# Kernel tuning notes

Hardware: AMD Instinct MI355X
Metric: run time of the kernel (lower is better)

The kernel has to match this reference:

```python
import jax, jax.numpy as jnp
import numpy as np

HD_DIM = 4096
BUNDLE_SIZE = 128
STRIDE = 128  # bundle_size - overlap, overlap = 0
EPS = 1e-8


def setup_inputs() -> dict:
    key = jax.random.key(0)
    k1, k2 = jax.random.split(key)
    inputs = jax.random.normal(k1, (4, 2048, HD_DIM), dtype=jnp.float32)
    # base vector ~ N(0, 1/sqrt(hd_dim)) as in RandomNormal(stddev=1/sqrt(hd_dim))
    base = jax.random.normal(k2, (HD_DIM,), dtype=jnp.float32) / jnp.sqrt(jnp.float32(HD_DIM))
    # position_weights initialized to decay_rate**i
    pos_w = jnp.power(jnp.float32(0.99), jnp.arange(BUNDLE_SIZE, dtype=jnp.float32))
    return {"inputs": inputs, "bundle_position_base": base, "position_weights": pos_w}


def reference(inputs, bundle_position_base, position_weights):
    B, S, D = inputs.shape
    nb = (S - BUNDLE_SIZE) // STRIDE + 1  # number of bundles

    # Cyclic-shift position vectors: pos[s, d] = base[(d - s) mod D]
    shifts = jnp.arange(BUNDLE_SIZE)
    idx = jnp.mod(jnp.arange(D)[None, :] - shifts[:, None], D)  # [bs, D]
    pos = bundle_position_base[idx]                              # [bs, D]
    w = jax.nn.softmax(position_weights)                         # [bs]
    pos = pos * w[:, None]

    # overlap=0 and S divisible by bundle_size -> bundles tile the sequence
    tok = inputs.reshape(B, nb, BUNDLE_SIZE, D)  # [B, nb, bs, D]

    # circular correlation: real(ifft(fft(tok) * conj(fft(pos))))
    # both operands real -> use rfft/irfft (identical math, half the work)
    tok_f = jnp.fft.rfft(tok, axis=-1)                 # [B, nb, bs, D//2+1]
    pos_f = jnp.conj(jnp.fft.rfft(pos, axis=-1))       # [bs, D//2+1]
    bound = jnp.fft.irfft(tok_f * pos_f[None, None], n=D, axis=-1)  # [B, nb, bs, D]

    bundle = jnp.sum(bound, axis=2)  # [B, nb, D]
    # tf.nn.l2_normalize: x * rsqrt(max(sum(x^2), eps))
    ssq = jnp.sum(bundle * bundle, axis=-1, keepdims=True)
    return (bundle * jax.lax.rsqrt(jnp.maximum(ssq, EPS))).astype(jnp.float32)
```

## Files before the change

kernel.cpp:

```cpp
#include <hip/hip_runtime.h>

#define D 4096
#define DM 4095
#define BS 128
#define NROW 64
#define QC 16
#define JC 8

#define ZSTR 520
#define PSTR 616

typedef __attribute__((ext_vector_type(8))) short bf16x8;
typedef __attribute__((ext_vector_type(4))) float f32x4;

__device__ __forceinline__ unsigned short f2bf(float f) {
  union { float f; unsigned int u; } v;
  v.f = f;
  const unsigned int r = v.u + 0x7fffu + ((v.u >> 16) & 1u);
  return (unsigned short)(r >> 16);
}

__global__ __launch_bounds__(256) void shift_k(const float* __restrict__ tok,
                                               const float* __restrict__ pw,
                                               float* __restrict__ part) {
  const int t = threadIdx.x;
  const int qc = blockIdx.x;
  const int row = blockIdx.y;

  __shared__ float wsh[BS];
  __shared__ float red[4];
  {
    const float v = (t < BS) ? pw[t] : -1e30f;
    float m = v;
#pragma unroll
    for (int o = 32; o > 0; o >>= 1) m = fmaxf(m, __shfl_xor(m, o));
    if ((t & 63) == 0) red[t >> 6] = m;
    __syncthreads();
    m = fmaxf(fmaxf(red[0], red[1]), fmaxf(red[2], red[3]));
    const float e = (t < BS) ? expf(v - m) : 0.f;
    float s = e;
#pragma unroll
    for (int o = 32; o > 0; o >>= 1) s += __shfl_xor(s, o);
    __syncthreads();
    if ((t & 63) == 0) red[t >> 6] = s;
    __syncthreads();
    s = red[0] + red[1] + red[2] + red[3];
    if (t < BS) wsh[t] = e / s;
    __syncthreads();
  }
  float wv[8];
#pragma unroll
  for (int j = 0; j < 8; ++j) wv[j] = wsh[(qc << 3) + j];

  const float4* tr = (const float4*)(tok + (size_t)row * (BS * D));
  float4 acc[4];
#pragma unroll
  for (int g = 0; g < 4; ++g) acc[g] = make_float4(0.f, 0.f, 0.f, 0.f);

#pragma unroll
  for (int qq = 0; qq < 2; ++qq) {
    const int q = (qc << 1) + qq;
    const float w0 = wv[4 * qq + 0], w1 = wv[4 * qq + 1];
    const float w2 = wv[4 * qq + 2], w3 = wv[4 * qq + 3];
#pragma unroll
    for (int g = 0; g < 4; ++g) {
      const int G = (t + (g << 8) + q) & 1023;
      const int G1 = (G + 1) & 1023;
      const size_t r0 = (size_t)(4 * q + 0) << 10;
      const size_t r1 = (size_t)(4 * q + 1) << 10;
      const size_t r2 = (size_t)(4 * q + 2) << 10;
      const size_t r3 = (size_t)(4 * q + 3) << 10;
      const float4 a0 = tr[r0 + G];
      const float4 a1 = tr[r1 + G], b1 = tr[r1 + G1];
      const float4 a2 = tr[r2 + G], b2 = tr[r2 + G1];
      const float4 a3 = tr[r3 + G], b3 = tr[r3 + G1];
      acc[g].x += w0 * a0.x; acc[g].y += w0 * a0.y;
      acc[g].z += w0 * a0.z; acc[g].w += w0 * a0.w;
      acc[g].x += w1 * a1.y; acc[g].y += w1 * a1.z;
      acc[g].z += w1 * a1.w; acc[g].w += w1 * b1.x;
      acc[g].x += w2 * a2.z; acc[g].y += w2 * a2.w;
      acc[g].z += w2 * b2.x; acc[g].w += w2 * b2.y;
      acc[g].x += w3 * a3.w; acc[g].y += w3 * b3.x;
      acc[g].z += w3 * b3.y; acc[g].w += w3 * b3.z;
    }
  }
  float4* pz = (float4*)(part + (size_t)(qc * NROW + row) * D);
#pragma unroll
  for (int g = 0; g < 4; ++g) pz[t + (g << 8)] = acc[g];
}

__global__ __launch_bounds__(256) void z_k(const float* __restrict__ part,
                                           unsigned short* __restrict__ zb) {
  const int t = threadIdx.x;
  const int mq = blockIdx.x;
  const int row = blockIdx.y;
  const int m0 = (mq << 10) + (t << 2);
  float4 s = make_float4(0.f, 0.f, 0.f, 0.f);
#pragma unroll
  for (int cc = 0; cc < QC; ++cc) {
    const float4 v = *(const float4*)(part + (size_t)(cc * NROW + row) * D + m0);
    s.x += v.x; s.y += v.y; s.z += v.z; s.w += v.w;
  }
  ushort4 o;
  o.x = f2bf(s.x); o.y = f2bf(s.y); o.z = f2bf(s.z); o.w = f2bf(s.w);
  *(ushort4*)(zb + (size_t)row * D + m0) = o;
}

__global__ __launch_bounds__(256) void corr_k(const unsigned short* __restrict__ zb,
                                              const float* __restrict__ base,
                                              float* __restrict__ braw) {
  __shared__ __align__(16) unsigned short zsh[16 * ZSTR];
  __shared__ __align__(16) unsigned short psh[8 * PSTR];
  const int t = threadIdx.x;
  const int jc = blockIdx.x;
  const int dg = blockIdx.y;
  const int rt = blockIdx.z;
  const int jb = jc << 9;
  const int d0b = dg << 6;

  {
    const int rr = t >> 4;
    const int c0 = (t & 15) << 5;
    const uint4* src =
        (const uint4*)(zb + (size_t)(rt * 16 + rr) * D + jb + c0);
    uint4* dst = (uint4*)(zsh + rr * ZSTR + c0);
    dst[0] = src[0];
    dst[1] = src[1];
    dst[2] = src[2];
    dst[3] = src[3];
  }
  {
    const int c0 = jb - d0b - 64 + 2 * D;
    for (int idx = t; idx < 8 * PSTR; idx += 256) {
      const int r = idx / PSTR;
      const int x = idx - r * PSTR;
      psh[idx] = f2bf(base[(c0 + r + x) & DM]);
    }
  }
  __syncthreads();

  const int lane = t & 63;
  const int w = t >> 6;
  const int dd = lane & 15;
  const int q = lane >> 4;
  const int a0 = 64 + (q << 3) - (w << 4) - dd;
  const int pr = a0 & 7;
  const int px = a0 - pr;
  const unsigned short* pA = psh + pr * PSTR + px;
  const unsigned short* pB = zsh + dd * ZSTR + (q << 3);

  f32x4 acc = {0.f, 0.f, 0.f, 0.f};
#pragma unroll
  for (int ks = 0; ks < 16; ++ks) {
    const bf16x8 af = *(const bf16x8*)(pA + (ks << 5));
    const bf16x8 bf = *(const bf16x8*)(pB + (ks << 5));
    acc = __builtin_amdgcn_mfma_f32_16x16x32_bf16(af, bf, acc, 0, 0, 0);
  }
  const int row = rt * 16 + dd;
  const int d = d0b + (w << 4) + (q << 2);
  float4 o = make_float4(acc[0], acc[1], acc[2], acc[3]);
  *(float4*)(braw + (size_t)(jc * NROW + row) * D + d) = o;
}

__global__ __launch_bounds__(1024) void norm_k(const float* __restrict__ braw,
                                               float* __restrict__ out) {
  const int t = threadIdx.x;
  const int row = blockIdx.x;
  const float4* b4 = (const float4*)braw;
  float4 s = make_float4(0.f, 0.f, 0.f, 0.f);
#pragma unroll
  for (int p = 0; p < JC; ++p) {
    const float4 v = b4[(size_t)(p * NROW + row) * (D / 4) + t];
    s.x += v.x; s.y += v.y; s.z += v.z; s.w += v.w;
  }
  float ssq = s.x * s.x + s.y * s.y + s.z * s.z + s.w * s.w;
#pragma unroll
  for (int o = 32; o > 0; o >>= 1) ssq += __shfl_xor(ssq, o);
  __shared__ float red[16];
  if ((t & 63) == 0) red[t >> 6] = ssq;
  __syncthreads();
  float tot = 0.f;
#pragma unroll
  for (int i = 0; i < 16; ++i) tot += red[i];
  const float sc = rsqrtf(fmaxf(tot, 1e-8f));
  float4 o;
  o.x = s.x * sc; o.y = s.y * sc; o.z = s.z * sc; o.w = s.w * sc;
  ((float4*)out)[(size_t)row * (D / 4) + t] = o;
}

extern "C" void kernel_launch(void* const* d_in, const int* in_sizes, int n_in,
                              void* d_out, int out_size, void* d_ws, size_t ws_size,
                              hipStream_t stream) {
  (void)in_sizes; (void)n_in; (void)out_size; (void)ws_size;
  const float* tok = (const float*)d_in[0];
  const float* base = (const float*)d_in[1];
  const float* pw = (const float*)d_in[2];
  float* out = (float*)d_out;

  float* part = (float*)d_ws;
  float* braw = part + (size_t)QC * NROW * D;
  unsigned short* zb =
      (unsigned short*)(braw + (size_t)JC * NROW * D);

  shift_k<<<dim3(QC, NROW), 256, 0, stream>>>(tok, pw, part);
  z_k<<<dim3(4, NROW), 256, 0, stream>>>(part, zb);
  corr_k<<<dim3(JC, 64, 4), 256, 0, stream>>>(zb, base, braw);
  norm_k<<<NROW, 1024, 0, stream>>>(braw, out);
}
```

Measured before the change: 208.5 us.

## Fuse shift-sum and partial reduction into one kernel with in-block LDS reduce

```diff
diff --git a/kernel.cpp b/kernel.cpp
--- a/kernel.cpp
+++ b/kernel.cpp
@@ -4,7 +4,6 @@
 #define DM 4095
 #define BS 128
 #define NROW 64
-#define QC 16
 #define JC 8
 
 #define ZSTR 520
@@ -20,15 +19,16 @@
   return (unsigned short)(r >> 16);
 }
 
-__global__ __launch_bounds__(256) void shift_k(const float* __restrict__ tok,
-                                               const float* __restrict__ pw,
-                                               float* __restrict__ part) {
+__global__ __launch_bounds__(256) void zshift_k(const float* __restrict__ tok,
+                                                const float* __restrict__ pw,
+                                                unsigned short* __restrict__ zb) {
   const int t = threadIdx.x;
-  const int qc = blockIdx.x;
+  const int mc = blockIdx.x;
   const int row = blockIdx.y;
 
   __shared__ float wsh[BS];
   __shared__ float red[4];
+  __shared__ float4 xsh[128];
   {
     const float v = (t < BS) ? pw[t] : -1e30f;
     float m = v;
@@ -48,62 +48,48 @@
     if (t < BS) wsh[t] = e / s;
     __syncthreads();
   }
-  float wv[8];
+
+  const int g = t & 127;
+  const int h = t >> 7;
+  const int og = (mc << 7) + g;
+  const float4* tr = (const float4*)(tok + (size_t)row * (BS * D));
+
+  float4 acc = make_float4(0.f, 0.f, 0.f, 0.f);
 #pragma unroll
-  for (int j = 0; j < 8; ++j) wv[j] = wsh[(qc << 3) + j];
-
-  const float4* tr = (const float4*)(tok + (size_t)row * (BS * D));
-  float4 acc[4];
-#pragma unroll
-  for (int g = 0; g < 4; ++g) acc[g] = make_float4(0.f, 0.f, 0.f, 0.f);
-
-#pragma unroll
-  for (int qq = 0; qq < 2; ++qq) {
-    const int q = (qc << 1) + qq;
-    const float w0 = wv[4 * qq + 0], w1 = wv[4 * qq + 1];
-    const float w2 = wv[4 * qq + 2], w3 = wv[4 * qq + 3];
-#pragma unroll
-    for (int g = 0; g < 4; ++g) {
-      const int G = (t + (g << 8) + q) & 1023;
-      const int G1 = (G + 1) & 1023;
-      const size_t r0 = (size_t)(4 * q + 0) << 10;
-      const size_t r1 = (size_t)(4 * q + 1) << 10;
-      const size_t r2 = (size_t)(4 * q + 2) << 10;
-      const size_t r3 = (size_t)(4 * q + 3) << 10;
-      const float4 a0 = tr[r0 + G];
-      const float4 a1 = tr[r1 + G], b1 = tr[r1 + G1];
-      const float4 a2 = tr[r2 + G], b2 = tr[r2 + G1];
-      const float4 a3 = tr[r3 + G], b3 = tr[r3 + G1];
-      acc[g].x += w0 * a0.x; acc[g].y += w0 * a0.y;
-      acc[g].z += w0 * a0.z; acc[g].w += w0 * a0.w;
-      acc[g].x += w1 * a1.y; acc[g].y += w1 * a1.z;
-      acc[g].z += w1 * a1.w; acc[g].w += w1 * b1.x;
-      acc[g].x += w2 * a2.z; acc[g].y += w2 * a2.w;
-      acc[g].z += w2 * b2.x; acc[g].w += w2 * b2.y;
-      acc[g].x += w3 * a3.w; acc[g].y += w3 * b3.x;
-      acc[g].z += w3 * b3.y; acc[g].w += w3 * b3.z;
-    }
+  for (int qq = 0; qq < 16; ++qq) {
+    const int q = (h << 4) + qq;
+    const float w0 = wsh[4 * q + 0], w1 = wsh[4 * q + 1];
+    const float w2 = wsh[4 * q + 2], w3 = wsh[4 * q + 3];
+    const int G = (og + q) & 1023;
+    const int G1 = (G + 1) & 1023;
+    const size_t r0 = (size_t)(4 * q + 0) << 10;
+    const size_t r1 = (size_t)(4 * q + 1) << 10;
+    const size_t r2 = (size_t)(4 * q + 2) << 10;
+    const size_t r3 = (size_t)(4 * q + 3) << 10;
+    const float4 a0 = tr[r0 + G];
+    const float4 a1 = tr[r1 + G], b1 = tr[r1 + G1];
+    const float4 a2 = tr[r2 + G], b2 = tr[r2 + G1];
+    const float4 a3 = tr[r3 + G], b3 = tr[r3 + G1];
+    acc.x += w0 * a0.x; acc.y += w0 * a0.y;
+    acc.z += w0 * a0.z; acc.w += w0 * a0.w;
+    acc.x += w1 * a1.y; acc.y += w1 * a1.z;
+    acc.z += w1 * a1.w; acc.w += w1 * b1.x;
+    acc.x += w2 * a2.z; acc.y += w2 * a2.w;
+    acc.z += w2 * b2.x; acc.w += w2 * b2.y;
+    acc.x += w3 * a3.w; acc.y += w3 * b3.x;
+    acc.z += w3 * b3.y; acc.w += w3 * b3.z;
   }
-  float4* pz = (float4*)(part + (size_t)(qc * NROW + row) * D);
-#pragma unroll
-  for (int g = 0; g < 4; ++g) pz[t + (g << 8)] = acc[g];
-}
-
-__global__ __launch_bounds__(256) void z_k(const float* __restrict__ part,
-                                           unsigned short* __restrict__ zb) {
-  const int t = threadIdx.x;
-  const int mq = blockIdx.x;
-  const int row = blockIdx.y;
-  const int m0 = (mq << 10) + (t << 2);
-  float4 s = make_float4(0.f, 0.f, 0.f, 0.f);
-#pragma unroll
-  for (int cc = 0; cc < QC; ++cc) {
-    const float4 v = *(const float4*)(part + (size_t)(cc * NROW + row) * D + m0);
-    s.x += v.x; s.y += v.y; s.z += v.z; s.w += v.w;
+  if (h) xsh[g] = acc;
+  __syncthreads();
+  if (!h) {
+    const float4 o = xsh[g];
+    ushort4 u;
+    u.x = f2bf(acc.x + o.x);
+    u.y = f2bf(acc.y + o.y);
+    u.z = f2bf(acc.z + o.z);
+    u.w = f2bf(acc.w + o.w);
+    *(ushort4*)(zb + (size_t)row * D + ((size_t)og << 2)) = u;
   }
-  ushort4 o;
-  o.x = f2bf(s.x); o.y = f2bf(s.y); o.z = f2bf(s.z); o.w = f2bf(s.w);
-  *(ushort4*)(zb + (size_t)row * D + m0) = o;
 }
 
 __global__ __launch_bounds__(256) void corr_k(const unsigned short* __restrict__ zb,
@@ -197,13 +183,10 @@
   const float* pw = (const float*)d_in[2];
   float* out = (float*)d_out;
 
-  float* part = (float*)d_ws;
-  float* braw = part + (size_t)QC * NROW * D;
-  unsigned short* zb =
-      (unsigned short*)(braw + (size_t)JC * NROW * D);
+  unsigned short* zb = (unsigned short*)d_ws;
+  float* braw = (float*)(zb + (size_t)NROW * D);
 
-  shift_k<<<dim3(QC, NROW), 256, 0, stream>>>(tok, pw, part);
-  z_k<<<dim3(4, NROW), 256, 0, stream>>>(part, zb);
+  zshift_k<<<dim3(8, NROW), 256, 0, stream>>>(tok, pw, zb);
   corr_k<<<dim3(JC, 64, 4), 256, 0, stream>>>(zb, base, braw);
   norm_k<<<NROW, 1024, 0, stream>>>(braw, out);
 }
```

New measurement: 205.8 us. Within noise of the previous version (-1.3%).
